# Optimization experiments

Measured on AMD Instinct MI355X. Metric: run time of the kernel, lower is better.

Reference implementation:

```python
import jax, jax.numpy as jnp
import numpy as np


def setup_inputs() -> dict:
    key = jax.random.key(0)
    k1, k2 = jax.random.split(key)
    B, C, H, W = 4, 32, 512, 512
    inp = jax.random.normal(k1, (B, C, H, W), dtype=jnp.float32)
    # flow displacements of a few pixels, realistic for optical-flow warping
    flow = jax.random.normal(k2, (B, 2, H, W), dtype=jnp.float32) * 8.0
    return {"input": inp, "flow": flow}


def reference(input, flow):
    B, C, H, W = input.shape
    dt = input.dtype
    # meshgrid: grid[:,0]=x coords, grid[:,1]=y coords
    gx = jnp.arange(W, dtype=dt)[None, None, :]          # [1,1,W]
    gy = jnp.arange(H, dtype=dt)[None, :, None]          # [1,H,1]
    x = jnp.clip(gx + flow[:, 0], 0.0, W - 1).reshape(-1)  # [B*H*W]
    y = jnp.clip(gy + flow[:, 1], 0.0, H - 1).reshape(-1)

    x0f = jnp.floor(x)
    y0f = jnp.floor(y)
    x1f = x0f + 1.0
    y1f = y0f + 1.0
    x0 = x0f.astype(jnp.int32)
    y0 = y0f.astype(jnp.int32)
    x1 = jnp.clip(x1f, 0.0, W - 1).astype(jnp.int32)
    y1 = jnp.clip(y1f, 0.0, H - 1).astype(jnp.int32)

    base = jnp.repeat(jnp.arange(B, dtype=jnp.int32) * (H * W), H * W)
    base_y0 = base + y0 * W
    base_y1 = base + y1 * W

    img_flat = jnp.transpose(input, (0, 2, 3, 1)).reshape(-1, C)  # [B*H*W, C]
    Ia = img_flat[base_y0 + x0]
    Ib = img_flat[base_y1 + x0]
    Ic = img_flat[base_y0 + x1]
    Id = img_flat[base_y1 + x1]

    # bilinear weights (note: weights use unclamped x1f/y1f, matching original)
    wa = ((x1f - x) * (y1f - y))[:, None]
    wb = ((x1f - x) * (y - y0f))[:, None]
    wc = ((x - x0f) * (y1f - y))[:, None]
    wd = ((x - x0f) * (y - y0f))[:, None]

    out = wa * Ia + wb * Ib + wc * Ic + wd * Id            # [B*H*W, C]
    return jnp.transpose(out.reshape(B, H, W, C), (0, 3, 1, 2))
```

## Files before the change

kernel.cpp:

```cpp
#include <hip/hip_runtime.h>


constexpr int B = 4, C = 32, H = 512, W = 512;
constexpr int HW = H * W;
constexpr int TILE = 64;
constexpr int APRON = 31;
constexpr int RH = 128;
constexpr int RW = 128;
constexpr int BUF = RH * RW;

typedef __attribute__((address_space(1))) const unsigned int gas_u32;
typedef __attribute__((address_space(3))) unsigned int las_u32;

__global__ __launch_bounds__(1024, 4) void warp_tile_kernel(
    const float* __restrict__ input,
    const float* __restrict__ flow,
    float* __restrict__ out)
{
    __shared__ float s[2 * BUF];

    int bid = blockIdx.x;
    int tx = bid & 7;
    int ty = (bid >> 3) & 7;
    int b  = bid >> 6;
    int tx0 = tx * TILE, ty0 = ty * TILE;

    int rx0 = tx0 - 32;
    int ry0 = ty0 - APRON;

    int tid  = (int)threadIdx.x;
    int lane = tid & 63;
    int wv   = tid >> 6;
    int cl   = tid & 63;
    int rl   = tid >> 6;

    int soff[4];
    int sr[4];
    {
        int lrow = lane >> 5;
        int lc   = (lane & 31) << 2;
        int gcol = min(max(rx0 + lc, 0), W - 4);
        #pragma unroll
        for (int i = 0; i < 4; ++i) {
            int r = 8 * wv + 2 * i;
            sr[i] = r;
            int grow = min(max(ry0 + r + lrow, 0), H - 1);
            soff[i] = grow * W + gcol;
        }
    }

    float wa[4], wb_[4], wc_[4], wd_[4];
    int a0[4], a1[4];
    int opix0 = (ty0 + rl) * W + tx0 + cl;

    #pragma unroll
    for (int p = 0; p < 4; ++p) {
        int h = ty0 + rl + 16 * p;
        int w = tx0 + cl;
        int pix = h * W + w;
        float fx = flow[(b * 2 + 0) * HW + pix];
        float fy = flow[(b * 2 + 1) * HW + pix];
        float x = fminf(fmaxf((float)w + fx, 0.0f), (float)(W - 1));
        float y = fminf(fmaxf((float)h + fy, 0.0f), (float)(H - 1));
        float x0f = floorf(x), y0f = floorf(y);
        int x0 = (int)x0f, y0 = (int)y0f;
        int y1 = min(y0 + 1, H - 1);
        float dx = x - x0f, dy = y - y0f;
        wa[p]  = (1.f - dx) * (1.f - dy);
        wb_[p] = (1.f - dx) * dy;
        wc_[p] = dx * (1.f - dy);
        wd_[p] = dx * dy;
        int ax0 = x0 - rx0, ay0 = y0 - ry0, ay1 = y1 - ry0;
        bool inreg = (ax0 >= 0) && (ax0 <= RW - 2) && (ay0 >= 0) && (ay1 <= RH - 1);
        a0[p] = inreg ? (ay0 * RW + ax0) : -1;
        a1[p] = ay1 * RW + ax0;
    }

    const float* iplane = input + (size_t)b * C * HW;
    float* oplane = out + (size_t)b * C * HW;

    auto stage = [&](int c, int buf) {
        const float* gc = iplane + (size_t)c * HW;
        #pragma unroll
        for (int i = 0; i < 4; ++i) {
            __builtin_amdgcn_global_load_lds(
                (gas_u32*)(gc + soff[i]),
                (las_u32*)(&s[buf * BUF + sr[i] * RW]),
                16, 0, 0);
        }
    };

    stage(0, 0);
    __syncthreads();

    for (int c = 0; c < C; ++c) {
        if (c + 1 < C) stage(c + 1, (c + 1) & 1);

        int base = (c & 1) * BUF;
        float* oc = oplane + (size_t)c * HW;
        #pragma unroll
        for (int p = 0; p < 4; ++p) {
            float v;
            if (a0[p] >= 0) {
                int i0 = base + a0[p], i1 = base + a1[p];
                float v00 = s[i0], v01 = s[i0 + 1];
                float v10 = s[i1], v11 = s[i1 + 1];
                v = wa[p] * v00 + wc_[p] * v01 + wb_[p] * v10 + wd_[p] * v11;
            } else {
                int h = ty0 + rl + 16 * p;
                int w = tx0 + cl;
                int pix = h * W + w;
                float fx = flow[(b * 2 + 0) * HW + pix];
                float fy = flow[(b * 2 + 1) * HW + pix];
                float x = fminf(fmaxf((float)w + fx, 0.0f), (float)(W - 1));
                float y = fminf(fmaxf((float)h + fy, 0.0f), (float)(H - 1));
                float x0f = floorf(x), y0f = floorf(y);
                int x0 = (int)x0f, y0 = (int)y0f;
                int x1 = min(x0 + 1, W - 1), y1 = min(y0 + 1, H - 1);
                float dx = x - x0f, dy = y - y0f;
                const float* pch = iplane + (size_t)c * HW;
                v = (1.f - dx) * (1.f - dy) * pch[y0 * W + x0]
                  + (1.f - dx) * dy         * pch[y1 * W + x0]
                  + dx * (1.f - dy)         * pch[y0 * W + x1]
                  + dx * dy                 * pch[y1 * W + x1];
            }
            oc[opix0 + 16 * p * W] = v;
        }
        __syncthreads();
    }
}

extern "C" void kernel_launch(void* const* d_in, const int* in_sizes, int n_in,
                              void* d_out, int out_size, void* d_ws, size_t ws_size,
                              hipStream_t stream) {
    const float* input = (const float*)d_in[0];
    const float* flow  = (const float*)d_in[1];
    float* out = (float*)d_out;

    int grid = B * (H / TILE) * (W / TILE);
    warp_tile_kernel<<<grid, 1024, 0, stream>>>(input, flow, out);
}
```

Baseline: 251.7 us.

## Shrink tiles to 64x32 with a single LDS buffer and XCD-aware block remap

Halves the tile height and block size and drops LDS double buffering, so each block uses 48KB of shared memory instead of 128KB and several blocks can share a CU. The next channel's global-to-LDS stage is now issued after a barrier and overlapped with the current channel's output stores, using a vmcnt wait to sync. The block index is also permuted so neighbouring tiles land on the same XCD for L2 reuse. In exchange, each block has less prefetch depth and proportionally more apron rows to load per output pixel.

```diff
diff --git a/kernel.cpp b/kernel.cpp
--- a/kernel.cpp
+++ b/kernel.cpp
@@ -3,27 +3,28 @@
 
 constexpr int B = 4, C = 32, H = 512, W = 512;
 constexpr int HW = H * W;
-constexpr int TILE = 64;
+constexpr int TW = 64, TH = 32;
 constexpr int APRON = 31;
-constexpr int RH = 128;
+constexpr int RH = 96;
 constexpr int RW = 128;
-constexpr int BUF = RH * RW;
 
 typedef __attribute__((address_space(1))) const unsigned int gas_u32;
 typedef __attribute__((address_space(3))) unsigned int las_u32;
 
-__global__ __launch_bounds__(1024, 4) void warp_tile_kernel(
+__global__ __launch_bounds__(512, 4) void warp_tile_kernel(
     const float* __restrict__ input,
     const float* __restrict__ flow,
     float* __restrict__ out)
 {
-    __shared__ float s[2 * BUF];
+    __shared__ float s[RH * RW];
 
-    int bid = blockIdx.x;
+    int bid0 = (int)blockIdx.x;
+    int bid = (bid0 & 7) * 64 + (bid0 >> 3);
+
     int tx = bid & 7;
-    int ty = (bid >> 3) & 7;
-    int b  = bid >> 6;
-    int tx0 = tx * TILE, ty0 = ty * TILE;
+    int ty = (bid >> 3) & 15;
+    int b  = bid >> 7;
+    int tx0 = tx * TW, ty0 = ty * TH;
 
     int rx0 = tx0 - 32;
     int ry0 = ty0 - APRON;
@@ -34,15 +35,15 @@
     int cl   = tid & 63;
     int rl   = tid >> 6;
 
-    int soff[4];
-    int sr[4];
+    int soff[6];
+    int sr[6];
     {
         int lrow = lane >> 5;
         int lc   = (lane & 31) << 2;
         int gcol = min(max(rx0 + lc, 0), W - 4);
         #pragma unroll
-        for (int i = 0; i < 4; ++i) {
-            int r = 8 * wv + 2 * i;
+        for (int i = 0; i < 6; ++i) {
+            int r = 12 * wv + 2 * i;
             sr[i] = r;
             int grow = min(max(ry0 + r + lrow, 0), H - 1);
             soff[i] = grow * W + gcol;
@@ -55,7 +56,7 @@
 
     #pragma unroll
     for (int p = 0; p < 4; ++p) {
-        int h = ty0 + rl + 16 * p;
+        int h = ty0 + rl + 8 * p;
         int w = tx0 + cl;
         int pix = h * W + w;
         float fx = flow[(b * 2 + 0) * HW + pix];
@@ -79,35 +80,30 @@
     const float* iplane = input + (size_t)b * C * HW;
     float* oplane = out + (size_t)b * C * HW;
 
-    auto stage = [&](int c, int buf) {
+    auto stage = [&](int c) {
         const float* gc = iplane + (size_t)c * HW;
         #pragma unroll
-        for (int i = 0; i < 4; ++i) {
+        for (int i = 0; i < 6; ++i) {
             __builtin_amdgcn_global_load_lds(
                 (gas_u32*)(gc + soff[i]),
-                (las_u32*)(&s[buf * BUF + sr[i] * RW]),
+                (las_u32*)(&s[sr[i] * RW]),
                 16, 0, 0);
         }
     };
 
-    stage(0, 0);
+    stage(0);
     __syncthreads();
 
     for (int c = 0; c < C; ++c) {
-        if (c + 1 < C) stage(c + 1, (c + 1) & 1);
-
-        int base = (c & 1) * BUF;
-        float* oc = oplane + (size_t)c * HW;
+        float v[4];
         #pragma unroll
         for (int p = 0; p < 4; ++p) {
-            float v;
             if (a0[p] >= 0) {
-                int i0 = base + a0[p], i1 = base + a1[p];
-                float v00 = s[i0], v01 = s[i0 + 1];
-                float v10 = s[i1], v11 = s[i1 + 1];
-                v = wa[p] * v00 + wc_[p] * v01 + wb_[p] * v10 + wd_[p] * v11;
+                float v00 = s[a0[p]],  v01 = s[a0[p] + 1];
+                float v10 = s[a1[p]],  v11 = s[a1[p] + 1];
+                v[p] = wa[p] * v00 + wc_[p] * v01 + wb_[p] * v10 + wd_[p] * v11;
             } else {
-                int h = ty0 + rl + 16 * p;
+                int h = ty0 + rl + 8 * p;
                 int w = tx0 + cl;
                 int pix = h * W + w;
                 float fx = flow[(b * 2 + 0) * HW + pix];
@@ -119,14 +115,31 @@
                 int x1 = min(x0 + 1, W - 1), y1 = min(y0 + 1, H - 1);
                 float dx = x - x0f, dy = y - y0f;
                 const float* pch = iplane + (size_t)c * HW;
-                v = (1.f - dx) * (1.f - dy) * pch[y0 * W + x0]
-                  + (1.f - dx) * dy         * pch[y1 * W + x0]
-                  + dx * (1.f - dy)         * pch[y0 * W + x1]
-                  + dx * dy                 * pch[y1 * W + x1];
+                v[p] = (1.f - dx) * (1.f - dy) * pch[y0 * W + x0]
+                     + (1.f - dx) * dy         * pch[y1 * W + x0]
+                     + dx * (1.f - dy)         * pch[y0 * W + x1]
+                     + dx * dy                 * pch[y1 * W + x1];
             }
-            oc[opix0 + 16 * p * W] = v;
         }
-        __syncthreads();
+
+        asm volatile("s_waitcnt lgkmcnt(0)" ::: "memory");
+        __builtin_amdgcn_sched_barrier(0);
+        __builtin_amdgcn_s_barrier();
+        __builtin_amdgcn_sched_barrier(0);
+
+        if (c + 1 < C) stage(c + 1);
+
+        float* oc = oplane + (size_t)c * HW;
+        #pragma unroll
+        for (int p = 0; p < 4; ++p)
+            oc[opix0 + 8 * p * W] = v[p];
+
+        if (c + 1 < C) {
+            asm volatile("s_waitcnt vmcnt(4)" ::: "memory");
+            __builtin_amdgcn_sched_barrier(0);
+            __builtin_amdgcn_s_barrier();
+            __builtin_amdgcn_sched_barrier(0);
+        }
     }
 }
 
@@ -137,6 +150,6 @@
     const float* flow  = (const float*)d_in[1];
     float* out = (float*)d_out;
 
-    int grid = B * (H / TILE) * (W / TILE);
-    warp_tile_kernel<<<grid, 1024, 0, stream>>>(input, flow, out);
+    int grid = B * (H / TH) * (W / TW);
+    warp_tile_kernel<<<grid, 512, 0, stream>>>(input, flow, out);
 }
```

Measured after the change: 271.1 us. +7.7%, slower.
